# Kernel optimization log

Hardware: AMD Instinct MI355X
Metric: run time of the kernel (lower is better)

The kernel has to match this reference:

```python
import jax, jax.numpy as jnp
import numpy as np

EPS = 1.1920929e-07  # torch RMSNorm default eps = finfo(fp32).eps
NUM_HEADS = 8
UP_HEAD = 64
ROPE_HEAD = 32
TOP_K = 4
HIDDEN = 512
INTER = 256
DQ = 256
DKV = 128
N_EXPERTS = 16
B, S = 2, 2048


def _rmsnorm(x, w):
    return x * jax.lax.rsqrt(jnp.mean(x * x, axis=-1, keepdims=True) + EPS) * w


def _rope(x):
    # x: [B, h, S, D] with D = ROPE_HEAD; rotate-half RoPE, base 10000
    D = x.shape[-1]
    s = x.shape[-2]
    inv_freq = 1.0 / (10000.0 ** (jnp.arange(0, D, 2, dtype=jnp.float32) / D))
    freqs = jnp.outer(jnp.arange(s, dtype=jnp.float32), inv_freq)  # [S, D/2]
    emb = jnp.concatenate([freqs, freqs], axis=-1)  # [S, D]
    cos, sin = jnp.cos(emb), jnp.sin(emb)
    x1, x2 = x[..., : D // 2], x[..., D // 2:]
    rot = jnp.concatenate([-x2, x1], axis=-1)
    return x * cos + rot * sin


def _swiglu(x, wg, wu, wd):
    return (jax.nn.silu(x @ wg) * (x @ wu)) @ wd


def setup_inputs() -> dict:
    key = jax.random.key(0)
    ks = jax.random.split(key, 18)
    sd = 0.02
    inp = {
        "hidden_states": jax.random.normal(ks[0], (B, S, HIDDEN), jnp.float32),
        "w_in_norm": jnp.ones((HIDDEN,), jnp.float32),
        "w_dq": sd * jax.random.normal(ks[1], (HIDDEN, DQ), jnp.float32),
        "w_qnorm": jnp.ones((DQ,), jnp.float32),
        "w_uq": sd * jax.random.normal(ks[2], (DQ, NUM_HEADS * (UP_HEAD + ROPE_HEAD)), jnp.float32),
        "w_dkv": sd * jax.random.normal(ks[3], (HIDDEN, DKV + ROPE_HEAD), jnp.float32),
        "w_kvnorm": jnp.ones((DKV,), jnp.float32),
        "w_ukv": sd * jax.random.normal(ks[4], (DKV, NUM_HEADS * UP_HEAD * 2), jnp.float32),
        "w_o": sd * jax.random.normal(ks[5], (NUM_HEADS * UP_HEAD, HIDDEN), jnp.float32),
        "w_post_norm": jnp.ones((HIDDEN,), jnp.float32),
        "w_gate": sd * jax.random.normal(ks[6], (HIDDEN, N_EXPERTS), jnp.float32),
        "sh_wg": sd * jax.random.normal(ks[7], (HIDDEN, INTER), jnp.float32),
        "sh_wu": sd * jax.random.normal(ks[8], (HIDDEN, INTER), jnp.float32),
        "sh_wd": sd * jax.random.normal(ks[9], (INTER, HIDDEN), jnp.float32),
        "r_wg": sd * jax.random.normal(ks[10], (N_EXPERTS, HIDDEN, INTER), jnp.float32),
        "r_wu": sd * jax.random.normal(ks[11], (N_EXPERTS, HIDDEN, INTER), jnp.float32),
        "r_wd": sd * jax.random.normal(ks[12], (N_EXPERTS, INTER, HIDDEN), jnp.float32),
    }
    return inp


def reference(hidden_states, w_in_norm, w_dq, w_qnorm, w_uq, w_dkv, w_kvnorm,
              w_ukv, w_o, w_post_norm, w_gate, sh_wg, sh_wu, sh_wd,
              r_wg, r_wu, r_wd):
    b, s, h = hidden_states.shape
    # ---- MLA attention block ----
    residual = hidden_states
    x = _rmsnorm(hidden_states, w_in_norm)
    c_q = x @ w_dq                                             # [B,S,Dq]
    qcr = _rmsnorm(c_q, w_qnorm) @ w_uq                        # [B,S,nh*(uh+rh)]
    qcr = qcr.reshape(b, s, NUM_HEADS, UP_HEAD + ROPE_HEAD).transpose(0, 2, 1, 3)
    q_c, q_r = qcr[..., :UP_HEAD], qcr[..., UP_HEAD:]
    ckv_kr = x @ w_dkv                                         # [B,S,Dkv+rh]
    c_kv, k_r = ckv_kr[..., :DKV], ckv_kr[..., DKV:]
    k_r = k_r[:, None, :, :]                                   # [B,1,S,rh]
    kv = (_rmsnorm(c_kv, w_kvnorm) @ w_ukv).reshape(b, s, NUM_HEADS, 2 * UP_HEAD).transpose(0, 2, 1, 3)
    k_c, v = kv[..., :UP_HEAD], kv[..., UP_HEAD:]
    q = jnp.concatenate([q_c, _rope(q_r)], axis=-1)            # [B,nh,S,96]
    k = jnp.concatenate([k_c, jnp.broadcast_to(_rope(k_r), (b, NUM_HEADS, s, ROPE_HEAD))], axis=-1)
    scale = 1.0 / jnp.sqrt(jnp.float32(UP_HEAD + ROPE_HEAD))
    attn = jax.nn.softmax(jnp.einsum('bhqd,bhkd->bhqk', q, k) * scale, axis=-1)
    o = jnp.einsum('bhqk,bhkd->bhqd', attn, v).transpose(0, 2, 1, 3).reshape(b, s, NUM_HEADS * UP_HEAD)
    x = o @ w_o + residual
    # ---- MoE block ----
    residual = x
    x = _rmsnorm(x, w_post_norm)
    x2 = x.reshape(-1, h)                                      # [T,H]
    shared = _swiglu(x2, sh_wg, sh_wu, sh_wd)                  # [T,H]
    scores = jax.nn.sigmoid(x2 @ w_gate)                       # [T,E]
    tw, ti = jax.lax.top_k(scores, TOP_K)                      # [T,k]
    tw = tw / jnp.sum(tw, axis=-1, keepdims=True)
    # combine[t,e] = routing weight of expert e for token t (0 if not selected)
    combine = jnp.sum(jax.nn.one_hot(ti, N_EXPERTS, dtype=x2.dtype) * tw[..., None], axis=1)  # [T,E]
    g = jnp.einsum('th,ehi->tei', x2, r_wg)
    u = jnp.einsum('th,ehi->tei', x2, r_wu)
    y = jnp.einsum('tei,eih->teh', jax.nn.silu(g) * u, r_wd)   # per-expert SwiGLU outputs
    routed = jnp.einsum('teh,te->th', y, combine)
    return (shared + routed).reshape(b, s, h) + residual
```

## Files before the change

### kernel.cpp

```cpp
#include <hip/hip_runtime.h>
#include <hip/hip_bf16.h>
#include <math.h>

typedef float f32x4 __attribute__((ext_vector_type(4)));
typedef short s16x8 __attribute__((ext_vector_type(8)));

constexpr int Tt = 4096;
constexpr int NEn = 16;
constexpr float EPSf = 1.1920929e-07f;
constexpr int CVT_BLOCKS = 7312;

__device__ __forceinline__ short f2b(float f) {
    union { __hip_bfloat16 h; short s; } u;
    u.h = __float2bfloat16(f);
    return u.s;
}
__device__ __forceinline__ float b2f(short s) {
    union { float f; unsigned u; } v;
    v.u = ((unsigned)(unsigned short)s) << 16;
    return v.f;
}

constexpr size_t alg(size_t x) { return (x + 15) & ~(size_t)15; }
constexpr size_t OFF_CQKV = 0;
constexpr size_t OFF_QCR  = alg(OFF_CQKV + (size_t)Tt * 416);
constexpr size_t OFF_KVB  = alg(OFF_QCR  + (size_t)Tt * 768);
constexpr size_t OFF_R2   = alg(OFF_KVB  + (size_t)Tt * 1024);
constexpr size_t OFF_TOKE = alg(OFF_R2   + (size_t)Tt * 512);
constexpr size_t OFF_TOKW = alg(OFF_TOKE + (size_t)Tt * 4);
constexpr size_t OFF_EWT  = alg(OFF_TOKW + (size_t)Tt * 4);
constexpr size_t OFF_ECNT = alg(OFF_EWT  + (size_t)NEn * Tt);
constexpr size_t OFF_ETOK = alg(OFF_ECNT + 64);
constexpr size_t OFF_PO   = 0;
constexpr size_t OFF_PL   = (size_t)16 * 2048 * 4 * 64 / 2;
constexpr size_t OFF_XNB   = alg(OFF_ETOK + (size_t)NEn * Tt);
constexpr size_t OFF_CQNB  = alg(OFF_XNB   + (size_t)Tt * 512 / 2);
constexpr size_t OFF_CKVNB = alg(OFF_CQNB  + (size_t)Tt * 256 / 2);
constexpr size_t OFF_QB    = alg(OFF_CKVNB + (size_t)Tt * 128 / 2);
constexpr size_t OFF_KB    = alg(OFF_QB    + (size_t)16 * 2048 * 96 / 2);
constexpr size_t OFF_VBT   = alg(OFF_KB    + (size_t)16 * 2048 * 96 / 2);
constexpr size_t OFF_XN2B  = alg(OFF_VBT   + (size_t)16 * 64 * 2048 / 2);
constexpr size_t OFF_GACT  = alg(OFF_XN2B  + (size_t)Tt * 512 / 2);
constexpr size_t OFF_EACT  = alg(OFF_GACT  + (size_t)Tt * 256 / 2);
constexpr size_t OFF_WQKVT = alg(OFF_EACT  + (size_t)16384 * 256 / 2);
constexpr size_t OFF_WUQT  = alg(OFF_WQKVT + (size_t)416 * 512 / 2);
constexpr size_t OFF_WUKVT = alg(OFF_WUQT  + (size_t)768 * 256 / 2);
constexpr size_t OFF_WOT   = alg(OFF_WUKVT + (size_t)1024 * 128 / 2);
constexpr size_t OFF_SHWGT = alg(OFF_WOT   + (size_t)512 * 512 / 2);
constexpr size_t OFF_SHWUT = alg(OFF_SHWGT + (size_t)256 * 512 / 2);
constexpr size_t OFF_SHWDT = alg(OFF_SHWUT + (size_t)256 * 512 / 2);
constexpr size_t OFF_RWGT  = alg(OFF_SHWDT + (size_t)512 * 256 / 2);
constexpr size_t OFF_RWUT  = alg(OFF_RWGT  + (size_t)16 * 256 * 512 / 2);
constexpr size_t OFF_RWDT  = alg(OFF_RWUT  + (size_t)16 * 256 * 512 / 2);

struct CvtTab {
    const float* src[11];
    short* dst[11];
    int K[11], N[11], end[11];
};

__global__ __launch_bounds__(256)
void k_cvt_rms(CvtTab tab, const float* __restrict__ in, const float* __restrict__ w,
               short* __restrict__ outB, int* __restrict__ ecnt) {
    __shared__ float t[32][33];
    __shared__ float xs[512];
    __shared__ float red[256];
    int bid = blockIdx.x, tid = threadIdx.x;
    if (bid < CVT_BLOCKS) {
        int i = 0;
        while (bid >= tab.end[i]) ++i;
        int tloc = bid - (i ? tab.end[i - 1] : 0);
        int K = tab.K[i], N = tab.N[i];
        int ntiles = N >> 5, perE = ntiles * (K >> 5);
        int e = tloc / perE, rem = tloc - e * perE;
        int k0 = (rem / ntiles) << 5, n0 = (rem % ntiles) << 5;
        size_t eo = (size_t)e * K * N;
        const float* src = tab.src[i];
        short* dst = tab.dst[i];
        int c = tid & 31, r = tid >> 5;
#pragma unroll
        for (int q = 0; q < 4; ++q)
            t[r + 8 * q][c] = src[eo + (size_t)(k0 + r + 8 * q) * N + n0 + c];
        __syncthreads();
#pragma unroll
        for (int q = 0; q < 4; ++q)
            dst[eo + (size_t)(n0 + r + 8 * q) * K + k0 + c] = f2b(t[c][r + 8 * q]);
    } else {
        int row = bid - CVT_BLOCKS;
        if (row == 0 && tid < 16) ecnt[tid] = 0;
        const float* ip = in + (size_t)row * 512;
        float ss = 0.f;
        for (int i = tid; i < 512; i += 256) { float v = ip[i]; xs[i] = v; ss += v * v; }
        red[tid] = ss; __syncthreads();
        for (int s = 128; s > 0; s >>= 1) { if (tid < s) red[tid] += red[tid + s]; __syncthreads(); }
        float sc = rsqrtf(red[0] / 512.f + EPSf);
        for (int i = tid; i < 512; i += 256) outB[(size_t)row * 512 + i] = f2b(xs[i] * sc * w[i]);
    }
}

__global__ void k_rms2(const float* __restrict__ cqkv, const float* __restrict__ wq, short* __restrict__ cqnb,
                       const float* __restrict__ wkv, short* __restrict__ ckvnb, short* __restrict__ kb) {
    int row = blockIdx.x, tid = threadIdx.x;
    if (row >= 2 * Tt) {
        int g2 = (row - 2 * Tt) * 256 + tid;
        int d2 = g2 & 31;
        int rs = g2 >> 5;
        int srow = rs & 2047;
        int bh = rs >> 11;
        int b = bh >> 3;
        int t = b * 2048 + srow;
        int fi = d2 & 15;
        float ang = (float)srow * __expf(-((float)(2 * fi) / 32.f) * 9.210340371976184f);
        float s, c; __sincosf(ang, &s, &c);
        float x = cqkv[(size_t)t * 416 + 384 + d2];
        float r = (d2 < 16) ? -cqkv[(size_t)t * 416 + 384 + d2 + 16]
                            :  cqkv[(size_t)t * 416 + 384 + d2 - 16];
        kb[((size_t)(bh * 2048 + srow)) * 96 + 64 + d2] = f2b(x * c + r * s);
        return;
    }
    __shared__ float xs[256];
    __shared__ float red[256];
    const float* ip; const float* w; short* ob; int D, outStride, r;
    if (row < Tt) { r = row;      ip = cqkv + (size_t)r * 416;       w = wq;  ob = cqnb;  D = 256; outStride = 256; }
    else          { r = row - Tt; ip = cqkv + (size_t)r * 416 + 256; w = wkv; ob = ckvnb; D = 128; outStride = 128; }
    float ss = 0.f;
    for (int i = tid; i < D; i += 256) { float v = ip[i]; xs[i] = v; ss += v * v; }
    red[tid] = ss; __syncthreads();
    for (int s = 128; s > 0; s >>= 1) { if (tid < s) red[tid] += red[tid + s]; __syncthreads(); }
    float sc = rsqrtf(red[0] / (float)D + EPSf);
    for (int i = tid; i < D; i += 256) ob[(size_t)r * outStride + i] = f2b(xs[i] * sc * w[i]);
}

__global__ __launch_bounds__(256)
void k_rms_router(const float* __restrict__ r2, const float* __restrict__ wpost,
                  const float* __restrict__ wg,
                  short* __restrict__ xn2b, int4* __restrict__ toke, float4* __restrict__ tokw) {
    int t = blockIdx.x, tid = threadIdx.x;
    __shared__ float xs[512];
    __shared__ float red[256];
    __shared__ float part[16][17];
    __shared__ float sc[16];
    const float* ip = r2 + (size_t)t * 512;
    float ss = 0.f;
    for (int i = tid; i < 512; i += 256) { float v = ip[i]; xs[i] = v; ss += v * v; }
    red[tid] = ss; __syncthreads();
    for (int s = 128; s > 0; s >>= 1) { if (tid < s) red[tid] += red[tid + s]; __syncthreads(); }
    float scale = rsqrtf(red[0] / 512.f + EPSf);
    for (int i = tid; i < 512; i += 256) {
        float v = xs[i] * scale * wpost[i];
        xs[i] = v;
        xn2b[(size_t)t * 512 + i] = f2b(v);
    }
    __syncthreads();
    {
        int e = tid & 15, ch = tid >> 4;
        const float* wp = wg + (size_t)ch * 32 * 16 + e;
        float s = 0.f;
#pragma unroll 8
        for (int k = 0; k < 32; ++k) s = fmaf(xs[ch * 32 + k], wp[(size_t)k * 16], s);
        part[ch][e] = s;
    }
    __syncthreads();
    if (tid < 16) {
        float s = 0.f;
#pragma unroll
        for (int c = 0; c < 16; ++c) s += part[c][tid];
        sc[tid] = 1.f / (1.f + expf(-s));
    }
    __syncthreads();
    if (tid < 64) {
        int lane = tid, e = lane & 15;
        float scv = sc[e];
        unsigned sel = 0;
        float tw[4]; int ti[4];
#pragma unroll
        for (int kk = 0; kk < 4; ++kk) {
            float cand = ((sel >> e) & 1u) ? -1e30f : scv;
            float mx = cand;
            mx = fmaxf(mx, __shfl_xor(mx, 1));
            mx = fmaxf(mx, __shfl_xor(mx, 2));
            mx = fmaxf(mx, __shfl_xor(mx, 4));
            mx = fmaxf(mx, __shfl_xor(mx, 8));
            unsigned long long msk = __ballot(cand == mx);
            int bi = (__ffsll(msk) - 1) & 15;
            tw[kk] = mx; ti[kk] = bi;
            sel |= 1u << bi;
        }
        if (lane == 0) {
            float inv = 1.f / (tw[0] + tw[1] + tw[2] + tw[3]);
            toke[t] = make_int4(ti[0], ti[1], ti[2], ti[3]);
            tokw[t] = make_float4(tw[0] * inv, tw[1] * inv, tw[2] * inv, tw[3] * inv);
        }
    }
}

__global__ __launch_bounds__(512)
void k_mgemm0(const short* __restrict__ A, const short* __restrict__ BT,
              float* __restrict__ C, int N, int K) {
    __shared__ __align__(16) short As[64 * 64];
    __shared__ __align__(16) short Bs[64 * 64];
    int tid = threadIdx.x;
    int w = tid >> 6, l = tid & 63, g = l >> 4, li = l & 15;
    int wm = w >> 1, wn = w & 1;
    int m0 = blockIdx.y * 64, n0 = blockIdx.x * 64;
    f32x4 acc[2] = {};
    for (int k0 = 0; k0 < K; k0 += 64) {
        __syncthreads();
        {
            int row = tid >> 3, ch = tid & 7;
            *(int4*)&As[row * 64 + ((ch ^ (row & 7)) * 8)] =
                *(const int4*)(A + (size_t)(m0 + row) * K + k0 + 8 * ch);
            int4 v = {0, 0, 0, 0};
            if (n0 + row < N) v = *(const int4*)(BT + (size_t)(n0 + row) * K + k0 + 8 * ch);
            *(int4*)&Bs[row * 64 + ((ch ^ (row & 7)) * 8)] = v;
        }
        __syncthreads();
#pragma unroll
        for (int kc = 0; kc < 2; ++kc) {
            int row = wm * 16 + li;
            s16x8 af = *(const s16x8*)&As[row * 64 + (((4 * kc + g) ^ (li & 7)) * 8)];
#pragma unroll
            for (int nt = 0; nt < 2; ++nt) {
                int n = wn * 32 + nt * 16 + li;
                s16x8 bf = *(const s16x8*)&Bs[n * 64 + (((4 * kc + g) ^ (li & 7)) * 8)];
                acc[nt] = __builtin_amdgcn_mfma_f32_16x16x32_bf16(af, bf, acc[nt], 0, 0, 0);
            }
        }
    }
#pragma unroll
    for (int nt = 0; nt < 2; ++nt)
#pragma unroll
        for (int r = 0; r < 4; ++r) {
            int gm = m0 + wm * 16 + 4 * g + r;
            int gn = n0 + wn * 32 + nt * 16 + li;
            if (gn < N) C[(size_t)gm * N + gn] = acc[nt][r];
        }
}

__global__ __launch_bounds__(512)
void k_upproj(const short* __restrict__ cqnb, const short* __restrict__ wuqT,
              short* __restrict__ qb,
              const short* __restrict__ ckvnb, const short* __restrict__ wukvT,
              short* __restrict__ kb, short* __restrict__ vbt) {
    __shared__ __align__(16) short As[64 * 64];
    __shared__ __align__(16) short Bs[64 * 64];
    int tid = threadIdx.x;
    int w = tid >> 6, l = tid & 63, g = l >> 4, li = l & 15;
    int wm = w >> 1, wn = w & 1;
    bool isQ = blockIdx.x < 12;
    const short* A  = isQ ? cqnb : ckvnb;
    const short* BT = isQ ? wuqT : wukvT;
    int N = isQ ? 768 : 1024;
    int K = isQ ? 256 : 128;
    int n0 = (isQ ? blockIdx.x : blockIdx.x - 12) * 64;
    int m0 = blockIdx.y * 64;
    f32x4 acc[2] = {};
    for (int k0 = 0; k0 < K; k0 += 64) {
        __syncthreads();
        {
            int row = tid >> 3, ch = tid & 7;
            *(int4*)&As[row * 64 + ((ch ^ (row & 7)) * 8)] =
                *(const int4*)(A + (size_t)(m0 + row) * K + k0 + 8 * ch);
            int4 v = {0, 0, 0, 0};
            if (n0 + row < N) v = *(const int4*)(BT + (size_t)(n0 + row) * K + k0 + 8 * ch);
            *(int4*)&Bs[row * 64 + ((ch ^ (row & 7)) * 8)] = v;
        }
        __syncthreads();
#pragma unroll
        for (int kc = 0; kc < 2; ++kc) {
            int row = wm * 16 + li;
            s16x8 af = *(const s16x8*)&As[row * 64 + (((4 * kc + g) ^ (li & 7)) * 8)];
#pragma unroll
            for (int nt = 0; nt < 2; ++nt) {
                int n = wn * 32 + nt * 16 + li;
                s16x8 bf = *(const s16x8*)&Bs[n * 64 + (((4 * kc + g) ^ (li & 7)) * 8)];
                acc[nt] = __builtin_amdgcn_mfma_f32_16x16x32_bf16(af, bf, acc[nt], 0, 0, 0);
            }
        }
    }
    const float scale = 0.14724389f;
#pragma unroll
    for (int r = 0; r < 4; ++r) {
        int gm = m0 + wm * 16 + 4 * g + r;
        int b = gm >> 11, srow = gm & 2047;
        int c0 = n0 + wn * 32 + li;
        float v0 = acc[0][r], v1 = acc[1][r];
        if (isQ) {
            int h = c0 / 96, dd0 = c0 - h * 96;
            int bh = b * 8 + h;
            size_t qoff = ((size_t)(bh * 2048 + srow)) * 96;
            if (dd0 >= 64) {
                int fi = dd0 - 64;
                float ang = (float)srow * __expf(-((float)(2 * fi) / 32.f) * 9.210340371976184f);
                float s, c; __sincosf(ang, &s, &c);
                qb[qoff + 64 + fi] = f2b((v0 * c - v1 * s) * scale);
                qb[qoff + 80 + fi] = f2b((v1 * c + v0 * s) * scale);
            } else {
                qb[qoff + dd0]      = f2b(v0 * scale);
                qb[qoff + dd0 + 16] = f2b(v1 * scale);
            }
        } else {
#pragma unroll
            for (int nt = 0; nt < 2; ++nt) {
                int gn = c0 + nt * 16;
                float v = nt ? v1 : v0;
                int h = gn >> 7, dd = gn & 127;
                int bh = b * 8 + h;
                if (dd < 64)
                    kb[((size_t)(bh * 2048 + srow)) * 96 + dd] = f2b(v);
                else
                    vbt[(size_t)bh * 64 * 2048 + (size_t)(dd - 64) * 2048 + srow] = f2b(v);
            }
        }
    }
}

__global__ __launch_bounds__(512)
void k_wo_gemm(const short* __restrict__ po, const float* __restrict__ pl,
               const short* __restrict__ BT, float* __restrict__ C,
               const float* __restrict__ add) {
    constexpr int N = 512, K = 512;
    __shared__ __align__(16) short As[64 * 64];
    __shared__ __align__(16) short Bs[64 * 64];
    int tid = threadIdx.x;
    int w = tid >> 6, l = tid & 63, g = l >> 4, li = l & 15;
    int wm = w >> 1, wn = w & 1;
    int m0 = blockIdx.y * 64, n0 = blockIdx.x * 64;
    int row = tid >> 3, ch = tid & 7;
    int t = m0 + row;
    int b = t >> 11, q = t & 2047;
    f32x4 acc[2] = {};
    for (int k0 = 0; k0 < K; k0 += 64) {
        int h = k0 >> 6;
        int bhq = (b * 8 + h) * 2048 + q;
        size_t pb = (size_t)bhq * 256 + 8 * ch;
        float4 l4 = *(const float4*)(pl + (size_t)bhq * 4);
        float inv = 1.f / (l4.x + l4.y + l4.z + l4.w);
        union { int4 v; short s[8]; } p0, p1, p2, p3, ov;
        p0.v = *(const int4*)(po + pb);
        p1.v = *(const int4*)(po + pb + 64);
        p2.v = *(const int4*)(po + pb + 128);
        p3.v = *(const int4*)(po + pb + 192);
#pragma unroll
        for (int i = 0; i < 8; ++i) {
            float os = b2f(p0.s[i]) + b2f(p1.s[i]) + b2f(p2.s[i]) + b2f(p3.s[i]);
            ov.s[i] = f2b(os * inv);
        }
        int4 bv = *(const int4*)(BT + (size_t)(n0 + row) * K + k0 + 8 * ch);
        __syncthreads();
        *(int4*)&As[row * 64 + ((ch ^ (row & 7)) * 8)] = ov.v;
        *(int4*)&Bs[row * 64 + ((ch ^ (row & 7)) * 8)] = bv;
        __syncthreads();
#pragma unroll
        for (int kc = 0; kc < 2; ++kc) {
            int rr = wm * 16 + li;
            s16x8 af = *(const s16x8*)&As[rr * 64 + (((4 * kc + g) ^ (li & 7)) * 8)];
#pragma unroll
            for (int nt = 0; nt < 2; ++nt) {
                int n = wn * 32 + nt * 16 + li;
                s16x8 bf = *(const s16x8*)&Bs[n * 64 + (((4 * kc + g) ^ (li & 7)) * 8)];
                acc[nt] = __builtin_amdgcn_mfma_f32_16x16x32_bf16(af, bf, acc[nt], 0, 0, 0);
            }
        }
    }
#pragma unroll
    for (int nt = 0; nt < 2; ++nt)
#pragma unroll
        for (int r = 0; r < 4; ++r) {
            int gm = m0 + wm * 16 + 4 * g + r;
            int gn = n0 + wn * 32 + nt * 16 + li;
            C[(size_t)gm * N + gn] = acc[nt][r] + add[(size_t)gm * N + gn];
        }
}

__global__ __launch_bounds__(256)
void k_attn(const short* __restrict__ qb, const short* __restrict__ kb,
            const short* __restrict__ vbt, short* __restrict__ po, float* __restrict__ pl) {
    __shared__ __align__(16) short Ks[64 * 100];
    __shared__ __align__(16) short Vs[80 * 64];
    int tid = threadIdx.x;
    int w = tid >> 6, l = tid & 63, g = l >> 4, li = l & 15;
    int blk = blockIdx.x;
    int bh = blk >> 6, rem = blk & 63;
    int qt = rem >> 2, ks = rem & 3;
    int qc0 = qt * 128 + w * 32;

    {
        const short one = 0x3F80;
        for (int i = tid; i < 16 * 64; i += 256)
            Vs[64 * 64 + i] = (i < 64) ? one : (short)0;
    }

    s16x8 qf[2][3];
#pragma unroll
    for (int j = 0; j < 2; ++j) {
        const short* qp = qb + (size_t)(bh * 2048 + qc0 + j * 16 + li) * 96;
#pragma unroll
        for (int c = 0; c < 3; ++c) qf[j][c] = *(const s16x8*)(qp + 32 * c + 8 * g);
    }

    f32x4 o[2][5] = {};
    const short* kbase = kb + (size_t)bh * 2048 * 96;
    const short* vbase = vbt + (size_t)bh * 64 * 2048;

    for (int t = 0; t < 8; ++t) {
        int koff = ks * 512 + t * 64;
        __syncthreads();
#pragma unroll
        for (int p = 0; p < 3; ++p) {
            int flat = p * 256 + tid;
            int key = flat / 12, u = flat % 12;
            *(int4*)&Ks[key * 100 + 8 * u] = *(const int4*)(kbase + (size_t)(koff + key) * 96 + 8 * u);
        }
#pragma unroll
        for (int p = 0; p < 2; ++p) {
            int flat = p * 256 + tid;
            int dim = flat >> 3, kc8 = flat & 7;
            int4 v = *(const int4*)(vbase + (size_t)dim * 2048 + koff + 8 * kc8);
            int sw = dim & 15;
            *(int2*)&Vs[dim * 64 + (((2 * kc8) ^ sw) * 4)]     = make_int2(v.x, v.y);
            *(int2*)&Vs[dim * 64 + (((2 * kc8 + 1) ^ sw) * 4)] = make_int2(v.z, v.w);
        }
        __syncthreads();

        f32x4 s[2][4];
#pragma unroll
        for (int kt = 0; kt < 4; ++kt) {
            f32x4 a0 = {}, a1 = {};
#pragma unroll
            for (int c = 0; c < 3; ++c) {
                s16x8 kf = *(const s16x8*)&Ks[(kt * 16 + li) * 100 + 32 * c + 8 * g];
                a0 = __builtin_amdgcn_mfma_f32_16x16x32_bf16(kf, qf[0][c], a0, 0, 0, 0);
                a1 = __builtin_amdgcn_mfma_f32_16x16x32_bf16(kf, qf[1][c], a1, 0, 0, 0);
            }
            s[0][kt] = a0; s[1][kt] = a1;
        }
#pragma unroll
        for (int j = 0; j < 2; ++j)
#pragma unroll
            for (int kt = 0; kt < 4; ++kt)
#pragma unroll
                for (int r = 0; r < 4; ++r) s[j][kt][r] = exp2f(s[j][kt][r]);
        s16x8 pf[2][2];
#pragma unroll
        for (int j = 0; j < 2; ++j)
#pragma unroll
            for (int kc = 0; kc < 2; ++kc) {
                s16x8 tt;
#pragma unroll
                for (int r = 0; r < 4; ++r) { tt[r] = f2b(s[j][2 * kc][r]); tt[4 + r] = f2b(s[j][2 * kc + 1][r]); }
                pf[j][kc] = tt;
            }
#pragma unroll
        for (int dt = 0; dt < 5; ++dt) {
            int dim = dt * 16 + li;
#pragma unroll
            for (int kc = 0; kc < 2; ++kc) {
                int2 a0 = *(const int2*)&Vs[dim * 64 + (((8 * kc + g) ^ li) * 4)];
                int2 a1 = *(const int2*)&Vs[dim * 64 + (((8 * kc + 4 + g) ^ li) * 4)];
                union { s16x8 v; int i[4]; } vf;
                vf.i[0] = a0.x; vf.i[1] = a0.y; vf.i[2] = a1.x; vf.i[3] = a1.y;
                o[0][dt] = __builtin_amdgcn_mfma_f32_16x16x32_bf16(vf.v, pf[0][kc], o[0][dt], 0, 0, 0);
                o[1][dt] = __builtin_amdgcn_mfma_f32_16x16x32_bf16(vf.v, pf[1][kc], o[1][dt], 0, 0, 0);
            }
        }
    }
#pragma unroll
    for (int j = 0; j < 2; ++j) {
        int qcol = qc0 + j * 16 + li;
        size_t qbase = ((size_t)(bh * 2048 + qcol) * 4 + ks) * 64;
#pragma unroll
        for (int dt = 0; dt < 4; ++dt) {
            union { short s[4]; int2 v; } pk;
#pragma unroll
            for (int r = 0; r < 4; ++r) pk.s[r] = f2b(o[j][dt][r]);
            *(int2*)(po + qbase + dt * 16 + 4 * g) = pk.v;
        }
        if (g == 0) pl[(size_t)(bh * 2048 + qcol) * 4 + ks] = o[j][4][0];
    }
}

__global__ __launch_bounds__(512)
void k_shexp_scatter(const short* __restrict__ X, const short* __restrict__ WGt,
                     const short* __restrict__ WUt, short* __restrict__ gact,
                     const int4* __restrict__ toke, const float4* __restrict__ tokw,
                     float* __restrict__ ewt, int* __restrict__ ecnt, int* __restrict__ etok) {
    __shared__ __align__(16) short As[64 * 64];
    __shared__ __align__(16) short Bg[64 * 64];
    __shared__ __align__(16) short Bu[64 * 64];
    __shared__ int lcnt[16];
    __shared__ int lbase[16];
    int bid = blockIdx.x, tid = threadIdx.x;
    if (bid < 256) {
        int w = tid >> 6, l = tid & 63, g = l >> 4, li = l & 15;
        int wm = w >> 1, wn = w & 1;
        int m0 = (bid & 63) * 64, n0 = (bid >> 6) * 64;
        f32x4 ag[2] = {}, au[2] = {};
        for (int k0 = 0; k0 < 512; k0 += 64) {
            __syncthreads();
            {
                int row = tid >> 3, ch = tid & 7;
                *(int4*)&As[row * 64 + ((ch ^ (row & 7)) * 8)] =
                    *(const int4*)(X + (size_t)(m0 + row) * 512 + k0 + 8 * ch);
                *(int4*)&Bg[row * 64 + ((ch ^ (row & 7)) * 8)] =
                    *(const int4*)(WGt + (size_t)(n0 + row) * 512 + k0 + 8 * ch);
                *(int4*)&Bu[row * 64 + ((ch ^ (row & 7)) * 8)] =
                    *(const int4*)(WUt + (size_t)(n0 + row) * 512 + k0 + 8 * ch);
            }
            __syncthreads();
#pragma unroll
            for (int kc = 0; kc < 2; ++kc) {
                int row = wm * 16 + li;
                s16x8 af = *(const s16x8*)&As[row * 64 + (((4 * kc + g) ^ (li & 7)) * 8)];
#pragma unroll
                for (int nt = 0; nt < 2; ++nt) {
                    int n = wn * 32 + nt * 16 + li;
                    s16x8 bg = *(const s16x8*)&Bg[n * 64 + (((4 * kc + g) ^ (li & 7)) * 8)];
                    s16x8 bu = *(const s16x8*)&Bu[n * 64 + (((4 * kc + g) ^ (li & 7)) * 8)];
                    ag[nt] = __builtin_amdgcn_mfma_f32_16x16x32_bf16(af, bg, ag[nt], 0, 0, 0);
                    au[nt] = __builtin_amdgcn_mfma_f32_16x16x32_bf16(af, bu, au[nt], 0, 0, 0);
                }
            }
        }
#pragma unroll
        for (int nt = 0; nt < 2; ++nt)
#pragma unroll
            for (int r = 0; r < 4; ++r) {
                int gm = m0 + (tid >> 6 >> 1) * 16 + 4 * ((tid & 63) >> 4) + r;
                int gn = n0 + ((tid >> 6) & 1) * 32 + nt * 16 + (tid & 15);
                float gv = ag[nt][r], uv = au[nt][r];
                gact[(size_t)gm * 256 + gn] = f2b(gv / (1.f + __expf(-gv)) * uv);
            }
    } else {
        int sb = bid - 256;
        bool act = tid < 256;
        int t = sb * 256 + (tid & 255);
        if (tid < 16) lcnt[tid] = 0;
        __syncthreads();
        int es[4]; float wv[4]; int ls[4] = {0, 0, 0, 0};
        if (act) {
            int4 e4 = toke[t];
            float4 w4 = tokw[t];
            es[0] = e4.x; es[1] = e4.y; es[2] = e4.z; es[3] = e4.w;
            wv[0] = w4.x; wv[1] = w4.y; wv[2] = w4.z; wv[3] = w4.w;
#pragma unroll
            for (int kk = 0; kk < 4; ++kk) ls[kk] = atomicAdd(&lcnt[es[kk]], 1);
        }
        __syncthreads();
        if (tid < 16) lbase[tid] = atomicAdd(&ecnt[tid], lcnt[tid]);
        __syncthreads();
        if (act) {
#pragma unroll
            for (int kk = 0; kk < 4; ++kk) {
                int slot = lbase[es[kk]] + ls[kk];
                etok[es[kk] * 4096 + slot] = t * 4 + kk;
                ewt[es[kk] * 4096 + slot] = wv[kk];
            }
        }
    }
}

__global__ __launch_bounds__(512)
void k_shd_moe1(const short* __restrict__ gact, const short* __restrict__ shwdT,
                float* __restrict__ outF, const float* __restrict__ r2,
                const short* __restrict__ X, const short* __restrict__ WGt,
                const short* __restrict__ WUt,
                const int* __restrict__ ecnt, const int* __restrict__ etok,
                short* __restrict__ eact) {
    __shared__ __align__(16) short smem[16384];
    __shared__ int toks[128];
    __shared__ int ecs[16];
    int bid = blockIdx.x, tid = threadIdx.x;
    int w = tid >> 6, l = tid & 63, g = l >> 4, li = l & 15;
    int wm = w >> 1, wn = w & 1;
    if (bid < 512) {
        short* As = smem;
        short* Bs = smem + 4096;
        constexpr int N = 512, K = 256;
        int n0 = (bid & 7) * 64, m0 = (bid >> 3) * 64;
        f32x4 acc[2] = {};
        for (int k0 = 0; k0 < K; k0 += 64) {
            __syncthreads();
            {
                int row = tid >> 3, ch = tid & 7;
                *(int4*)&As[row * 64 + ((ch ^ (row & 7)) * 8)] =
                    *(const int4*)(gact + (size_t)(m0 + row) * K + k0 + 8 * ch);
                *(int4*)&Bs[row * 64 + ((ch ^ (row & 7)) * 8)] =
                    *(const int4*)(shwdT + (size_t)(n0 + row) * K + k0 + 8 * ch);
            }
            __syncthreads();
#pragma unroll
            for (int kc = 0; kc < 2; ++kc) {
                int row = wm * 16 + li;
                s16x8 af = *(const s16x8*)&As[row * 64 + (((4 * kc + g) ^ (li & 7)) * 8)];
#pragma unroll
                for (int nt = 0; nt < 2; ++nt) {
                    int n = wn * 32 + nt * 16 + li;
                    s16x8 bf = *(const s16x8*)&Bs[n * 64 + (((4 * kc + g) ^ (li & 7)) * 8)];
                    acc[nt] = __builtin_amdgcn_mfma_f32_16x16x32_bf16(af, bf, acc[nt], 0, 0, 0);
                }
            }
        }
#pragma unroll
        for (int nt = 0; nt < 2; ++nt)
#pragma unroll
            for (int r = 0; r < 4; ++r) {
                int gm = m0 + wm * 16 + 4 * g + r;
                int gn = n0 + wn * 32 + nt * 16 + li;
                outF[(size_t)gm * N + gn] = acc[nt][r] + r2[(size_t)gm * N + gn];
            }
    } else {
        short* As = smem;
        short* Bg = smem + 8192;
        short* Bu = smem + 12288;
        if (tid < 16) ecs[tid] = ecnt[tid];
        __syncthreads();
        int lin = bid - 512;
        int virt = (lin & 7) * 72 + (lin >> 3);
        int tb = virt >> 2;
        int n0 = (virt & 3) * 64;
        int e = 0;
        for (; e < 16; ++e) { int n = (ecs[e] + 127) >> 7; if (tb < n) break; tb -= n; }
        if (e >= 16) return;
        int base = tb << 7;
        int rows = min(128, ecs[e] - base);
        if (tid < 128) toks[tid] = (tid < rows) ? etok[e * 4096 + base + tid] : -1;
        __syncthreads();
        const short* wgp = WGt + (size_t)e * 256 * 512;
        const short* wup = WUt + (size_t)e * 256 * 512;
        f32x4 ag[2][2] = {}, au[2][2] = {};
        for (int k0 = 0; k0 < 512; k0 += 64) {
            __syncthreads();
#pragma unroll
            for (int p = 0; p < 2; ++p) {
                int flat = p * 512 + tid;
                int row = flat >> 3, ch = flat & 7;
                int tk = toks[row];
                int4 v = {0, 0, 0, 0};
                if (tk >= 0) v = *(const int4*)(X + (size_t)(tk >> 2) * 512 + k0 + 8 * ch);
                *(int4*)&As[row * 64 + ((ch ^ (row & 7)) * 8)] = v;
            }
            {
                int n = tid >> 3, ch = tid & 7;
                *(int4*)&Bg[n * 64 + ((ch ^ (n & 7)) * 8)] = *(const int4*)(wgp + (size_t)(n0 + n) * 512 + k0 + 8 * ch);
                *(int4*)&Bu[n * 64 + ((ch ^ (n & 7)) * 8)] = *(const int4*)(wup + (size_t)(n0 + n) * 512 + k0 + 8 * ch);
            }
            __syncthreads();
#pragma unroll
            for (int kc = 0; kc < 2; ++kc) {
                s16x8 af[2], bg[2], bu[2];
#pragma unroll
                for (int mt = 0; mt < 2; ++mt) {
                    int row = wm * 32 + mt * 16 + li;
                    af[mt] = *(const s16x8*)&As[row * 64 + (((4 * kc + g) ^ (li & 7)) * 8)];
                }
#pragma unroll
                for (int nt = 0; nt < 2; ++nt) {
                    int n = wn * 32 + nt * 16 + li;
                    bg[nt] = *(const s16x8*)&Bg[n * 64 + (((4 * kc + g) ^ (li & 7)) * 8)];
                    bu[nt] = *(const s16x8*)&Bu[n * 64 + (((4 * kc + g) ^ (li & 7)) * 8)];
                }
#pragma unroll
                for (int mt = 0; mt < 2; ++mt)
#pragma unroll
                    for (int nt = 0; nt < 2; ++nt) {
                        ag[mt][nt] = __builtin_amdgcn_mfma_f32_16x16x32_bf16(af[mt], bg[nt], ag[mt][nt], 0, 0, 0);
                        au[mt][nt] = __builtin_amdgcn_mfma_f32_16x16x32_bf16(af[mt], bu[nt], au[mt][nt], 0, 0, 0);
                    }
            }
        }
#pragma unroll
        for (int mt = 0; mt < 2; ++mt)
#pragma unroll
            for (int nt = 0; nt < 2; ++nt)
#pragma unroll
                for (int r = 0; r < 4; ++r) {
                    int local = wm * 32 + mt * 16 + 4 * g + r;
                    if (local < rows) {
                        int entry = toks[local];
                        int gn = n0 + wn * 32 + nt * 16 + li;
                        float gv = ag[mt][nt][r], uv = au[mt][nt][r];
                        eact[(size_t)entry * 256 + gn] = f2b(gv / (1.f + __expf(-gv)) * uv);
                    }
                }
    }
}

__global__ __launch_bounds__(512)
void k_moe2m(const short* __restrict__ EA, const short* __restrict__ WDt,
             const int* __restrict__ ecnt, const int* __restrict__ etok,
             const float* __restrict__ ewt, float* __restrict__ oacc) {
    __shared__ int ecs[16];
    __shared__ __align__(16) short As[128 * 64];
    __shared__ __align__(16) short Bs[64 * 64];
    __shared__ int toks[128];
    __shared__ float wts[128];
    int tid = threadIdx.x;
    if (tid < 16) ecs[tid] = ecnt[tid];
    __syncthreads();
    int lin = blockIdx.x + 144 * blockIdx.y;
    int virt = (lin & 7) * 144 + (lin >> 3);
    int bid = virt >> 3;
    int n0 = (virt & 7) * 64;
    int e = 0;
    for (; e < 16; ++e) { int n = (ecs[e] + 127) >> 7; if (bid < n) break; bid -= n; }
    if (e >= 16) return;
    int base = bid << 7;
    int rows = min(128, ecs[e] - base);
    if (tid < 128) {
        toks[tid] = (tid < rows) ? etok[e * 4096 + base + tid] : -1;
        wts[tid]  = (tid < rows) ? ewt[e * 4096 + base + tid] : 0.f;
    }
    __syncthreads();
    int w = tid >> 6, l = tid & 63, g = l >> 4, li = l & 15;
    int wm = w >> 1, wn = w & 1;
    const short* wdp = WDt + (size_t)e * 512 * 256;
    f32x4 acc[2][2] = {};
    for (int k0 = 0; k0 < 256; k0 += 64) {
        __syncthreads();
#pragma unroll
        for (int p = 0; p < 2; ++p) {
            int flat = p * 512 + tid;
            int row = flat >> 3, ch = flat & 7;
            int tk = toks[row];
            int4 v = {0, 0, 0, 0};
            if (tk >= 0) v = *(const int4*)(EA + (size_t)tk * 256 + k0 + 8 * ch);
            *(int4*)&As[row * 64 + ((ch ^ (row & 7)) * 8)] = v;
        }
        {
            int n = tid >> 3, ch = tid & 7;
            *(int4*)&Bs[n * 64 + ((ch ^ (n & 7)) * 8)] = *(const int4*)(wdp + (size_t)(n0 + n) * 256 + k0 + 8 * ch);
        }
        __syncthreads();
#pragma unroll
        for (int kc = 0; kc < 2; ++kc) {
            s16x8 af[2], bf[2];
#pragma unroll
            for (int mt = 0; mt < 2; ++mt) {
                int row = wm * 32 + mt * 16 + li;
                af[mt] = *(const s16x8*)&As[row * 64 + (((4 * kc + g) ^ (li & 7)) * 8)];
            }
#pragma unroll
            for (int nt = 0; nt < 2; ++nt) {
                int n = wn * 32 + nt * 16 + li;
                bf[nt] = *(const s16x8*)&Bs[n * 64 + (((4 * kc + g) ^ (li & 7)) * 8)];
            }
#pragma unroll
            for (int mt = 0; mt < 2; ++mt)
#pragma unroll
                for (int nt = 0; nt < 2; ++nt)
                    acc[mt][nt] = __builtin_amdgcn_mfma_f32_16x16x32_bf16(af[mt], bf[nt], acc[mt][nt], 0, 0, 0);
        }
    }
#pragma unroll
    for (int mt = 0; mt < 2; ++mt)
#pragma unroll
        for (int nt = 0; nt < 2; ++nt)
#pragma unroll
            for (int r = 0; r < 4; ++r) {
                int local = wm * 32 + mt * 16 + 4 * g + r;
                if (local < rows) {
                    int tok = toks[local] >> 2;
                    int gn = n0 + wn * 32 + nt * 16 + li;
                    atomicAdd(&oacc[(size_t)tok * 512 + gn], acc[mt][nt][r] * wts[local]);
                }
            }
}

extern "C" void kernel_launch(void* const* d_in, const int* in_sizes, int n_in,
                              void* d_out, int out_size, void* d_ws, size_t ws_size,
                              hipStream_t stream) {
    const float* hs       = (const float*)d_in[0];
    const float* w_innorm = (const float*)d_in[1];
    const float* w_dq     = (const float*)d_in[2];
    const float* w_qnorm  = (const float*)d_in[3];
    const float* w_uq     = (const float*)d_in[4];
    const float* w_dkv    = (const float*)d_in[5];
    const float* w_kvnorm = (const float*)d_in[6];
    const float* w_ukv    = (const float*)d_in[7];
    const float* w_o      = (const float*)d_in[8];
    const float* w_post   = (const float*)d_in[9];
    const float* w_gate   = (const float*)d_in[10];
    const float* sh_wg    = (const float*)d_in[11];
    const float* sh_wu    = (const float*)d_in[12];
    const float* sh_wd    = (const float*)d_in[13];
    const float* r_wg     = (const float*)d_in[14];
    const float* r_wu     = (const float*)d_in[15];
    const float* r_wd     = (const float*)d_in[16];

    float* ws   = (float*)d_ws;
    float* cqkv = ws + OFF_CQKV;
    float* r2   = ws + OFF_R2;
    short* po   = (short*)(ws + OFF_PO);
    float* pl   = ws + OFF_PL;
    int4*  toke = (int4*)(ws + OFF_TOKE);
    float4* tokw = (float4*)(ws + OFF_TOKW);
    float* ewt  = ws + OFF_EWT;
    int*   ecnt = (int*)(ws + OFF_ECNT);
    int*   etok = (int*)(ws + OFF_ETOK);
    short* xnb   = (short*)(ws + OFF_XNB);
    short* cqnb  = (short*)(ws + OFF_CQNB);
    short* ckvnb = (short*)(ws + OFF_CKVNB);
    short* qb    = (short*)(ws + OFF_QB);
    short* kb    = (short*)(ws + OFF_KB);
    short* vbt   = (short*)(ws + OFF_VBT);
    short* xn2b  = (short*)(ws + OFF_XN2B);
    short* gact  = (short*)(ws + OFF_GACT);
    short* eact  = (short*)(ws + OFF_EACT);
    short* wqkvT = (short*)(ws + OFF_WQKVT);
    short* wuqT  = (short*)(ws + OFF_WUQT);
    short* wukvT = (short*)(ws + OFF_WUKVT);
    short* woT   = (short*)(ws + OFF_WOT);
    short* shwgT = (short*)(ws + OFF_SHWGT);
    short* shwuT = (short*)(ws + OFF_SHWUT);
    short* shwdT = (short*)(ws + OFF_SHWDT);
    short* rwgT  = (short*)(ws + OFF_RWGT);
    short* rwuT  = (short*)(ws + OFF_RWUT);
    short* rwdT  = (short*)(ws + OFF_RWDT);

    float* outF = (float*)d_out;

    CvtTab tab;
    const float* srcs[11] = { w_dq, w_dkv, w_uq, w_ukv, w_o, sh_wg, sh_wu, sh_wd, r_wg, r_wu, r_wd };
    short* dsts[11] = { wqkvT, wqkvT + (size_t)256 * 512, wuqT, wukvT, woT, shwgT, shwuT, shwdT, rwgT, rwuT, rwdT };
    int Ks_[11] = { 512, 512, 256, 128, 512, 512, 512, 256, 512, 512, 256 };
    int Ns_[11] = { 256, 160, 768, 1024, 512, 256, 256, 512, 256, 256, 512 };
    int Es_[11] = { 1, 1, 1, 1, 1, 1, 1, 1, 16, 16, 16 };
    int cum = 0;
    for (int i = 0; i < 11; ++i) {
        tab.src[i] = srcs[i]; tab.dst[i] = dsts[i];
        tab.K[i] = Ks_[i]; tab.N[i] = Ns_[i];
        cum += Es_[i] * (Ks_[i] >> 5) * (Ns_[i] >> 5);
        tab.end[i] = cum;
    }
    k_cvt_rms<<<CVT_BLOCKS + Tt, 256, 0, stream>>>(tab, hs, w_innorm, xnb, ecnt);

    k_mgemm0<<<dim3(7, 64), 512, 0, stream>>>(xnb, wqkvT, cqkv, 416, 512);
    k_rms2<<<2 * Tt + 4096, 256, 0, stream>>>(cqkv, w_qnorm, cqnb, w_kvnorm, ckvnb, kb);
    k_upproj<<<dim3(28, 64), 512, 0, stream>>>(cqnb, wuqT, qb, ckvnb, wukvT, kb, vbt);
    k_attn<<<1024, 256, 0, stream>>>(qb, kb, vbt, po, pl);
    k_wo_gemm<<<dim3(8, 64), 512, 0, stream>>>(po, pl, woT, r2, hs);
    k_rms_router<<<Tt, 256, 0, stream>>>(r2, w_post, w_gate, xn2b, toke, tokw);
    k_shexp_scatter<<<272, 512, 0, stream>>>(xn2b, shwgT, shwuT, gact, toke, tokw, ewt, ecnt, etok);
    k_shd_moe1<<<1088, 512, 0, stream>>>(gact, shwdT, outF, r2, xn2b, rwgT, rwuT, ecnt, etok, eact);
    k_moe2m<<<dim3(144, 8), 512, 0, stream>>>(eact, rwdT, ecnt, etok, ewt, outF);
}
```

Before: 201.3 us.

## Fuse k-rope into first GEMM epilogue and vectorize V LDS reads

The rotary embedding of the shared k-rope slice moves from extra blocks in k_rms2 into the epilogue of k_mgemm0. That GEMM already holds columns d and d+16 of the rope slice in registers (acc[0] and acc[1]), so no second global read of cqkv is needed and 4096 blocks drop from the k_rms2 launch. Separately, the attention V tile in LDS is re-laid out with a 72-element row pitch and an 8-element XOR swizzle. Each MFMA operand then comes from a single 16-byte LDS load instead of two 8-byte loads plus repacking. The risks are a more complex swizzle mapping that must match the write pattern, and scattered 2-byte global writes from the GEMM epilogue.

```diff
diff --git a/kernel.cpp b/kernel.cpp
--- a/kernel.cpp
+++ b/kernel.cpp
@@ -99,25 +99,8 @@
 }
 
 __global__ void k_rms2(const float* __restrict__ cqkv, const float* __restrict__ wq, short* __restrict__ cqnb,
-                       const float* __restrict__ wkv, short* __restrict__ ckvnb, short* __restrict__ kb) {
+                       const float* __restrict__ wkv, short* __restrict__ ckvnb) {
     int row = blockIdx.x, tid = threadIdx.x;
-    if (row >= 2 * Tt) {
-        int g2 = (row - 2 * Tt) * 256 + tid;
-        int d2 = g2 & 31;
-        int rs = g2 >> 5;
-        int srow = rs & 2047;
-        int bh = rs >> 11;
-        int b = bh >> 3;
-        int t = b * 2048 + srow;
-        int fi = d2 & 15;
-        float ang = (float)srow * __expf(-((float)(2 * fi) / 32.f) * 9.210340371976184f);
-        float s, c; __sincosf(ang, &s, &c);
-        float x = cqkv[(size_t)t * 416 + 384 + d2];
-        float r = (d2 < 16) ? -cqkv[(size_t)t * 416 + 384 + d2 + 16]
-                            :  cqkv[(size_t)t * 416 + 384 + d2 - 16];
-        kb[((size_t)(bh * 2048 + srow)) * 96 + 64 + d2] = f2b(x * c + r * s);
-        return;
-    }
     __shared__ float xs[256];
     __shared__ float red[256];
     const float* ip; const float* w; short* ob; int D, outStride, r;
@@ -196,7 +179,7 @@
 
 __global__ __launch_bounds__(512)
 void k_mgemm0(const short* __restrict__ A, const short* __restrict__ BT,
-              float* __restrict__ C, int N, int K) {
+              float* __restrict__ C, int N, int K, short* __restrict__ kb) {
     __shared__ __align__(16) short As[64 * 64];
     __shared__ __align__(16) short Bs[64 * 64];
     int tid = threadIdx.x;
@@ -235,6 +218,26 @@
             int gn = n0 + wn * 32 + nt * 16 + li;
             if (gn < N) C[(size_t)gm * N + gn] = acc[nt][r];
         }
+    if (n0 == 384 && wn == 0) {
+        int d2 = li;
+        float dec = __expf(-((float)(2 * d2) / 32.f) * 9.210340371976184f);
+#pragma unroll
+        for (int r = 0; r < 4; ++r) {
+            int gm = m0 + wm * 16 + 4 * g + r;
+            int b = gm >> 11, srow = gm & 2047;
+            float ang = (float)srow * dec;
+            float s, c; __sincosf(ang, &s, &c);
+            float x0 = acc[0][r], x1 = acc[1][r];
+            short s0 = f2b(x0 * c - x1 * s);
+            short s1 = f2b(x1 * c + x0 * s);
+#pragma unroll
+            for (int h = 0; h < 8; ++h) {
+                size_t off = ((size_t)((b * 8 + h) * 2048 + srow)) * 96;
+                kb[off + 64 + d2] = s0;
+                kb[off + 80 + d2] = s1;
+            }
+        }
+    }
 }
 
 __global__ __launch_bounds__(512)
@@ -377,7 +380,7 @@
 void k_attn(const short* __restrict__ qb, const short* __restrict__ kb,
             const short* __restrict__ vbt, short* __restrict__ po, float* __restrict__ pl) {
     __shared__ __align__(16) short Ks[64 * 100];
-    __shared__ __align__(16) short Vs[80 * 64];
+    __shared__ __align__(16) short Vs[80 * 72];
     int tid = threadIdx.x;
     int w = tid >> 6, l = tid & 63, g = l >> 4, li = l & 15;
     int blk = blockIdx.x;
@@ -387,8 +390,8 @@
 
     {
         const short one = 0x3F80;
-        for (int i = tid; i < 16 * 64; i += 256)
-            Vs[64 * 64 + i] = (i < 64) ? one : (short)0;
+        for (int i = tid; i < 16 * 72; i += 256)
+            Vs[64 * 72 + i] = (i < 72) ? one : (short)0;
     }
 
     s16x8 qf[2][3];
@@ -417,9 +420,13 @@
             int flat = p * 256 + tid;
             int dim = flat >> 3, kc8 = flat & 7;
             int4 v = *(const int4*)(vbase + (size_t)dim * 2048 + koff + 8 * kc8);
-            int sw = dim & 15;
-            *(int2*)&Vs[dim * 64 + (((2 * kc8) ^ sw) * 4)]     = make_int2(v.x, v.y);
-            *(int2*)&Vs[dim * 64 + (((2 * kc8 + 1) ^ sw) * 4)] = make_int2(v.z, v.w);
+            int m0 = 2 * kc8;
+            int c0 = ((m0 >> 3) << 2) | (m0 & 3);
+            int h4 = ((m0 >> 2) & 1) * 4;
+            int sw = dim & 7;
+            short* vrow = &Vs[dim * 72];
+            *(int2*)&vrow[((c0 ^ sw) * 8) + h4]       = make_int2(v.x, v.y);
+            *(int2*)&vrow[(((c0 + 1) ^ sw) * 8) + h4] = make_int2(v.z, v.w);
         }
         __syncthreads();
 
@@ -454,14 +461,12 @@
 #pragma unroll
         for (int dt = 0; dt < 5; ++dt) {
             int dim = dt * 16 + li;
+            int swd = dim & 7;
 #pragma unroll
             for (int kc = 0; kc < 2; ++kc) {
-                int2 a0 = *(const int2*)&Vs[dim * 64 + (((8 * kc + g) ^ li) * 4)];
-                int2 a1 = *(const int2*)&Vs[dim * 64 + (((8 * kc + 4 + g) ^ li) * 4)];
-                union { s16x8 v; int i[4]; } vf;
-                vf.i[0] = a0.x; vf.i[1] = a0.y; vf.i[2] = a1.x; vf.i[3] = a1.y;
-                o[0][dt] = __builtin_amdgcn_mfma_f32_16x16x32_bf16(vf.v, pf[0][kc], o[0][dt], 0, 0, 0);
-                o[1][dt] = __builtin_amdgcn_mfma_f32_16x16x32_bf16(vf.v, pf[1][kc], o[1][dt], 0, 0, 0);
+                s16x8 vf = *(const s16x8*)&Vs[dim * 72 + (((kc * 4 + g) ^ swd) * 8)];
+                o[0][dt] = __builtin_amdgcn_mfma_f32_16x16x32_bf16(vf, pf[0][kc], o[0][dt], 0, 0, 0);
+                o[1][dt] = __builtin_amdgcn_mfma_f32_16x16x32_bf16(vf, pf[1][kc], o[1][dt], 0, 0, 0);
             }
         }
     }
@@ -835,8 +840,8 @@
     }
     k_cvt_rms<<<CVT_BLOCKS + Tt, 256, 0, stream>>>(tab, hs, w_innorm, xnb, ecnt);
 
-    k_mgemm0<<<dim3(7, 64), 512, 0, stream>>>(xnb, wqkvT, cqkv, 416, 512);
-    k_rms2<<<2 * Tt + 4096, 256, 0, stream>>>(cqkv, w_qnorm, cqnb, w_kvnorm, ckvnb, kb);
+    k_mgemm0<<<dim3(7, 64), 512, 0, stream>>>(xnb, wqkvT, cqkv, 416, 512, kb);
+    k_rms2<<<2 * Tt, 256, 0, stream>>>(cqkv, w_qnorm, cqnb, w_kvnorm, ckvnb);
     k_upproj<<<dim3(28, 64), 512, 0, stream>>>(cqnb, wuqT, qb, ckvnb, wukvT, kb, vbt);
     k_attn<<<1024, 256, 0, stream>>>(qb, kb, vbt, po, pl);
     k_wo_gemm<<<dim3(8, 64), 512, 0, stream>>>(po, pl, woT, r2, hs);
```

Result: no change. 202.0 us (+0.4%).
